# Kernel tuning notes

Hardware: AMD Instinct MI355X
Metric: run time of the kernel (lower is better)

Reference implementation:

```python
import jax, jax.numpy as jnp
import numpy as np

HEAD_SIZE = 64
TOKEN_EMB = 768
BLOCK_SIZE = 4096


def setup_inputs() -> dict:
    key = jax.random.key(0)
    ks = jax.random.split(key, 7)
    s = 1.0 / np.sqrt(TOKEN_EMB)  # torch Linear default init scale
    x = jax.random.normal(ks[0], (4, BLOCK_SIZE, TOKEN_EMB), dtype=jnp.float32)
    Wk = jax.random.uniform(ks[1], (TOKEN_EMB, HEAD_SIZE), minval=-s, maxval=s, dtype=jnp.float32)
    bk = jax.random.uniform(ks[2], (HEAD_SIZE,), minval=-s, maxval=s, dtype=jnp.float32)
    Wq = jax.random.uniform(ks[3], (TOKEN_EMB, HEAD_SIZE), minval=-s, maxval=s, dtype=jnp.float32)
    bq = jax.random.uniform(ks[4], (HEAD_SIZE,), minval=-s, maxval=s, dtype=jnp.float32)
    Wv = jax.random.uniform(ks[5], (TOKEN_EMB, HEAD_SIZE), minval=-s, maxval=s, dtype=jnp.float32)
    bv = jax.random.uniform(ks[6], (HEAD_SIZE,), minval=-s, maxval=s, dtype=jnp.float32)
    return {"x": x, "Wk": Wk, "bk": bk, "Wq": Wq, "bq": bq, "Wv": Wv, "bv": bv}


def reference(x, Wk, bk, Wq, bq, Wv, bv):
    B, T, C = x.shape
    k = x @ Wk + bk  # [B, T, H]
    q = x @ Wq + bq  # [B, T, H]
    v = x @ Wv + bv  # [B, T, H]
    # NOTE: original computes k @ q^T (not q @ k^T) and scales by C**-0.5 with
    # C = token embedding size (not head size). Reproduce faithfully.
    scale = jnp.asarray(C, x.dtype) ** -0.5
    wei = jnp.einsum('bth,bsh->bts', k, q) * scale  # [B, T, T]
    causal = jnp.tril(jnp.ones((T, T), dtype=bool))
    wei = jnp.where(causal, wei, -jnp.inf)
    wei = jax.nn.softmax(wei, axis=-1)
    return jnp.einsum('bts,bsh->bth', wei, v)  # [B, T, H]
```

## Files before the change

### kernel.cpp

```cpp
#include <hip/hip_runtime.h>
#include <hip/hip_bf16.h>

#define T_SEQ 4096
#define C_EMB 768
#define HEAD  64

typedef short  short4v __attribute__((ext_vector_type(4)));
typedef short  short8  __attribute__((ext_vector_type(8)));
typedef float  floatx4 __attribute__((ext_vector_type(4)));
typedef unsigned int uint2v __attribute__((ext_vector_type(2)));

static __device__ __forceinline__ short f2bf(float v) {
    __hip_bfloat16 h = __float2bfloat16(v);
    return *reinterpret_cast<short*>(&h);
}


__global__ void wt_transpose_kernel(const float* __restrict__ Wk,
                                    const float* __restrict__ Wq,
                                    const float* __restrict__ Wv,
                                    short* __restrict__ Wf) {
    const int total = 12 * 24 * 64 * 8;
    for (int idx = blockIdx.x * blockDim.x + threadIdx.x; idx < total;
         idx += gridDim.x * blockDim.x) {
        int e    = idx & 7;
        int lane = (idx >> 3) & 63;
        int t    = idx >> 9;
        int kc   = t % 24;
        int j    = t / 24;
        int g    = j >> 2;
        int n    = (j & 3) * 16 + (lane & 15);
        int k    = kc * 32 + ((lane >> 4) & 3) * 8 + e;
        const float* W = (g == 0) ? Wk : (g == 1) ? Wq : Wv;
        Wf[idx] = f2bf(W[k * HEAD + n]);
    }
}

__global__ __launch_bounds__(512) void qkv_mfma(
    const float* __restrict__ x, const short* __restrict__ Wf,
    const float* __restrict__ bkp, const float* __restrict__ bqp,
    const float* __restrict__ bvp,
    short* __restrict__ Kf, short* __restrict__ Qf, short* __restrict__ Vf) {
    const float scale2 = 0.052058773f;
    __shared__ __align__(16) short xs[32][776];

    const int tid  = threadIdx.x;
    const int w    = tid >> 6;
    const int lane = tid & 63;
    const int ln15 = lane & 15, quad = lane >> 4;
    const int rows0 = blockIdx.x * 32;
    const int rw = (w & 1) * 16;
    const int jb = (w >> 1) * 3;

#pragma unroll
    for (int grp = 0; grp < 2; ++grp) {
        floatx4 stg[6];
#pragma unroll
        for (int i = 0; i < 6; ++i) {
            int o = (grp * 6 + i) * 2048 + tid * 4;
            int r = o / 768, col = o - r * 768;
            stg[i] = *(const floatx4*)(x + (size_t)(rows0 + r) * C_EMB + col);
        }
#pragma unroll
        for (int i = 0; i < 6; ++i) {
            int o = (grp * 6 + i) * 2048 + tid * 4;
            int r = o / 768, col = o - r * 768;
            unsigned p01, p23;
            asm("v_cvt_pk_bf16_f32 %0, %1, %2" : "=v"(p01) : "v"(stg[i][0]), "v"(stg[i][1]));
            asm("v_cvt_pk_bf16_f32 %0, %1, %2" : "=v"(p23) : "v"(stg[i][2]), "v"(stg[i][3]));
            *(uint2v*)&xs[r][col] = (uint2v){p01, p23};
        }
    }
    __syncthreads();

    const short* wp[3];
#pragma unroll
    for (int j0 = 0; j0 < 3; ++j0)
        wp[j0] = Wf + ((size_t)((jb + j0) * 24) * 64 + lane) * 8;

    floatx4 acc[3];
#pragma unroll
    for (int jj = 0; jj < 3; ++jj) acc[jj] = (floatx4){0.f, 0.f, 0.f, 0.f};

#pragma unroll
    for (int kc = 0; kc < 24; ++kc) {
        short8 a = *(const short8*)&xs[rw + ln15][kc * 32 + quad * 8];
        short8 wf[3];
#pragma unroll
        for (int jj = 0; jj < 3; ++jj)
            wf[jj] = *(const short8*)(wp[jj] + kc * 512);
#pragma unroll
        for (int jj = 0; jj < 3; ++jj)
            acc[jj] = __builtin_amdgcn_mfma_f32_16x16x32_bf16(a, wf[jj], acc[jj], 0, 0, 0);
    }
    __syncthreads();

    short* lds = &xs[0][0];
#pragma unroll
    for (int jj = 0; jj < 3; ++jj) {
        int j  = jb + jj;
        int g  = j >> 2;
        int nl = (j & 3) * 16 + ln15;
        float bias = (g == 0 ? bkp : g == 1 ? bqp : bvp)[nl];
#pragma unroll
        for (int r = 0; r < 4; ++r) {
            int rloc = rw + quad * 4 + r;
            float v = acc[jj][r] + bias;
            int off;
            short val;
            if (g == 2) {
                val = f2bf(v);
                off = 4096 + ((nl >> 4) << 9) +
                      ((((rloc >> 3) & 3) << 4) | (nl & 15)) * 8 + (rloc & 7);
            } else {
                val = (g == 0) ? f2bf(v * scale2) : f2bf(v);
                int tr = rloc & 15, kh = nl >> 5;
                int hq = (nl >> 3) & 3, he = nl & 7;
                off = (g << 11) + (((rloc >> 4) * 2 + kh) << 9) +
                      (tr | (hq << 4)) * 8 + he;
            }
            lds[off] = val;
        }
    }
    __syncthreads();

    {
        int bb = rows0 >> 12, s = rows0 & 4095;
        size_t vbase = ((size_t)bb << 18) +
                       ((size_t)((s >> 6) * 8 + ((s >> 5) & 1)) << 9);
#pragma unroll
        for (int cc = 0; cc < 2; ++cc) {
            int i = (cc * 512 + tid) * 8;
            if (i < 6144) {
                short8 d = *(const short8*)&lds[i];
                if (i < 2048)
                    *(short8*)(Kf + (size_t)rows0 * 64 + i) = d;
                else if (i < 4096)
                    *(short8*)(Qf + (size_t)rows0 * 64 + (i - 2048)) = d;
                else {
                    int iv = i - 4096;
                    *(short8*)(Vf + vbase + (size_t)(iv >> 9) * 1024 + (iv & 511)) = d;
                }
            }
        }
    }
}

__global__ __launch_bounds__(64) void attn_part(
    const short* __restrict__ Kf, const short* __restrict__ Qf,
    const short* __restrict__ Vf, float* __restrict__ Opart,
    float* __restrict__ lpart) {
    __shared__ __align__(16) short Ps[32][72];

    int lane = threadIdx.x & 63;
    int ln15 = lane & 15, quad = lane >> 4;
    int g32 = blockIdx.x, c = blockIdx.y, b = blockIdx.z;
    int dtile = g32 >> 1;
    int lo = c * 8;
    if (lo > dtile) return;
    int hi = min(dtile, lo + 7);
    int base = g32 * 32;

    short8 bk[2][2];
    {
        const short* kfp = Kf + ((size_t)(b * 256 + g32 * 2) * 2) * 512 + lane * 8;
#pragma unroll
        for (int tg = 0; tg < 2; ++tg)
#pragma unroll
            for (int kh = 0; kh < 2; ++kh)
                bk[tg][kh] = *(const short8*)(kfp + (tg * 2 + kh) * 512);
    }

    floatx4 o[2][4];
#pragma unroll
    for (int tg = 0; tg < 2; ++tg)
#pragma unroll
        for (int hb = 0; hb < 4; ++hb) o[tg][hb] = (floatx4){0.f, 0.f, 0.f, 0.f};
    float ls[2] = {0.f, 0.f};

    const short* qfp = Qf + ((size_t)(b * 256 + lo * 4) * 2) * 512 + lane * 8;
    const short* vfp = Vf + ((size_t)b << 18) + (size_t)lo * 8 * 512 + lane * 8;

    short8 aqA[4][2], bvA[4][2], aqB[4][2], bvB[4][2];
#pragma unroll
    for (int sb = 0; sb < 4; ++sb)
#pragma unroll
        for (int kh = 0; kh < 2; ++kh)
            aqA[sb][kh] = *(const short8*)(qfp + (sb * 2 + kh) * 512);
#pragma unroll
    for (int hb = 0; hb < 4; ++hb)
#pragma unroll
        for (int kh = 0; kh < 2; ++kh)
            bvA[hb][kh] = *(const short8*)(vfp + (hb * 2 + kh) * 512);

    auto tile_step = [&](short8 (&aq)[4][2], short8 (&bv)[4][2],
                         short8 (&aqn)[4][2], short8 (&bvn)[4][2], int st) {
        if (st < hi) {
            int ti = st + 1 - lo;
#pragma unroll
            for (int sb = 0; sb < 4; ++sb)
#pragma unroll
                for (int kh = 0; kh < 2; ++kh)
                    aqn[sb][kh] = *(const short8*)(qfp + (size_t)ti * 4096 +
                                                   (sb * 2 + kh) * 512);
#pragma unroll
            for (int hb = 0; hb < 4; ++hb)
#pragma unroll
                for (int kh = 0; kh < 2; ++kh)
                    bvn[hb][kh] = *(const short8*)(vfp + (size_t)ti * 4096 +
                                                   (hb * 2 + kh) * 512);
        }

        floatx4 sacc[4][2];
#pragma unroll
        for (int sb = 0; sb < 4; ++sb)
#pragma unroll
            for (int tg = 0; tg < 2; ++tg) {
                floatx4 z = (floatx4){0.f, 0.f, 0.f, 0.f};
                z = __builtin_amdgcn_mfma_f32_16x16x32_bf16(aq[sb][0], bk[tg][0], z, 0, 0, 0);
                z = __builtin_amdgcn_mfma_f32_16x16x32_bf16(aq[sb][1], bk[tg][1], z, 0, 0, 0);
                sacc[sb][tg] = z;
            }

        bool diag = (st == dtile);
        int s0 = st * 64;
#pragma unroll
        for (int tg = 0; tg < 2; ++tg) {
            int tgl = base + tg * 16 + ln15;
#pragma unroll
            for (int sb = 0; sb < 4; ++sb) {
                float pv4[4];
#pragma unroll
                for (int r = 0; r < 4; ++r) {
                    float p = __builtin_amdgcn_exp2f(sacc[sb][tg][r]);
                    if (diag) {
                        int sg = s0 + sb * 16 + quad * 4 + r;
                        p = (sg > tgl) ? 0.f : p;
                    }
                    pv4[r] = p;
                }
                ls[tg] += (pv4[0] + pv4[1]) + (pv4[2] + pv4[3]);
                unsigned a01, a23;
                asm("v_cvt_pk_bf16_f32 %0, %1, %2" : "=v"(a01) : "v"(pv4[0]), "v"(pv4[1]));
                asm("v_cvt_pk_bf16_f32 %0, %1, %2" : "=v"(a23) : "v"(pv4[2]), "v"(pv4[3]));
                *(uint2v*)&Ps[tg * 16 + ln15][sb * 16 + quad * 4] = (uint2v){a01, a23};
            }
        }
        __asm__ volatile("s_waitcnt lgkmcnt(0)" ::: "memory");
        short8 ap[2][2];
#pragma unroll
        for (int tg = 0; tg < 2; ++tg) {
            ap[tg][0] = *(const short8*)&Ps[tg * 16 + ln15][quad * 8];
            ap[tg][1] = *(const short8*)&Ps[tg * 16 + ln15][32 + quad * 8];
        }

#pragma unroll
        for (int tg = 0; tg < 2; ++tg)
#pragma unroll
            for (int hb = 0; hb < 4; ++hb) {
                o[tg][hb] = __builtin_amdgcn_mfma_f32_16x16x32_bf16(ap[tg][0], bv[hb][0], o[tg][hb], 0, 0, 0);
                o[tg][hb] = __builtin_amdgcn_mfma_f32_16x16x32_bf16(ap[tg][1], bv[hb][1], o[tg][hb], 0, 0, 0);
            }
    };

#pragma unroll
    for (int it = 0; it < 8; it += 2) {
        if (lo + it > hi) break;
        tile_step(aqA, bvA, aqB, bvB, lo + it);
        if (lo + it + 1 > hi) break;
        tile_step(aqB, bvB, aqA, bvA, lo + it + 1);
    }

    float* op = Opart + ((size_t)(b * 8 + c) << 12) * HEAD;
    float* lp = lpart + ((size_t)(b * 8 + c) << 12);

#pragma unroll
    for (int tg = 0; tg < 2; ++tg) {
        float v = ls[tg];
        v += __shfl_xor(v, 16, 64);
        v += __shfl_xor(v, 32, 64);
        if (quad == 0)
            lp[base + tg * 16 + ln15] = v;
    }
#pragma unroll
    for (int tg = 0; tg < 2; ++tg)
#pragma unroll
        for (int r = 0; r < 4; ++r) {
            int t = base + tg * 16 + quad * 4 + r;
#pragma unroll
            for (int hb = 0; hb < 4; ++hb)
                op[(size_t)t * HEAD + hb * 16 + ln15] = o[tg][hb][r];
        }
}

__global__ __launch_bounds__(256) void attn_div(
    const float* __restrict__ Opart, const float* __restrict__ lpart,
    float* __restrict__ out) {
    int idx = blockIdx.x * 256 + threadIdx.x;
    int h = idx & 63;
    int t = (idx >> 6) & 4095;
    int b = idx >> 18;
    int nch = (t >> 9) + 1;
    float os = 0.f, l = 0.f;
    for (int c = 0; c < nch; ++c) {
        size_t s = (size_t)(b * 8 + c) << 12;
        os += Opart[(s + t) * HEAD + h];
        l  += lpart[s + t];
    }
    out[idx] = os / l;
}

extern "C" void kernel_launch(void* const* d_in, const int* in_sizes, int n_in,
                              void* d_out, int out_size, void* d_ws, size_t ws_size,
                              hipStream_t stream) {
    const int XSZ = 4 * T_SEQ * C_EMB;
    const int WSZ = C_EMB * HEAD;
    const int BSZ = HEAD;
    const float* x = nullptr;
    const float* W[3] = {nullptr, nullptr, nullptr};
    const float* B[3] = {nullptr, nullptr, nullptr};
    int iw = 0, ib = 0;
    for (int i = 0; i < n_in; ++i) {
        if (in_sizes[i] == XSZ) x = (const float*)d_in[i];
        else if (in_sizes[i] == WSZ && iw < 3) W[iw++] = (const float*)d_in[i];
        else if (in_sizes[i] == BSZ && ib < 3) B[ib++] = (const float*)d_in[i];
    }

    short* ws = (short*)d_ws;
    short* Kf = ws;
    short* Qf = Kf + (size_t)4 * T_SEQ * HEAD;
    short* Vf = Qf + (size_t)4 * T_SEQ * HEAD;
    short* Wf = Vf + (size_t)4 * HEAD * T_SEQ;
    float* Opart = (float*)(Wf + (size_t)3 * HEAD * C_EMB);
    float* lpart = Opart + (size_t)32 * T_SEQ * HEAD;

    wt_transpose_kernel<<<96, 256, 0, stream>>>(W[0], W[1], W[2], Wf);
    qkv_mfma<<<512, 512, 0, stream>>>(x, Wf, B[0], B[1], B[2], Kf, Qf, Vf);
    attn_part<<<dim3(128, 8, 4), 64, 0, stream>>>(Kf, Qf, Vf, Opart, lpart);
    attn_div<<<4096, 256, 0, stream>>>(Opart, lpart, (float*)d_out);
}
```

Measured before the change: 142.2 us.

## Split attention into 16 key chunks and drop register double-buffering

Halves the key-chunk size per attention workgroup (4 tiles instead of 8) and doubles the grid along the chunk axis, so more single-wave workgroups run in parallel and each finishes sooner. The manual ping-pong prefetch of Q/V fragments is replaced by a plain loop that loads each tile's fragments just before use. The reduction kernel now sums up to 16 partials per row, which doubles the partial-output workspace and the traffic through attn_div. Removing the prefetch may expose global load latency, but it lowers register pressure.

Result: faster. 137.2 us (-3.5%).

```diff
diff --git a/kernel.cpp b/kernel.cpp
--- a/kernel.cpp
+++ b/kernel.cpp
@@ -156,9 +156,9 @@
     int ln15 = lane & 15, quad = lane >> 4;
     int g32 = blockIdx.x, c = blockIdx.y, b = blockIdx.z;
     int dtile = g32 >> 1;
-    int lo = c * 8;
+    int lo = c * 4;
     if (lo > dtile) return;
-    int hi = min(dtile, lo + 7);
+    int hi = min(dtile, lo + 3);
     int base = g32 * 32;
 
     short8 bk[2][2];
@@ -181,35 +181,18 @@
     const short* qfp = Qf + ((size_t)(b * 256 + lo * 4) * 2) * 512 + lane * 8;
     const short* vfp = Vf + ((size_t)b << 18) + (size_t)lo * 8 * 512 + lane * 8;
 
-    short8 aqA[4][2], bvA[4][2], aqB[4][2], bvB[4][2];
-#pragma unroll
-    for (int sb = 0; sb < 4; ++sb)
-#pragma unroll
-        for (int kh = 0; kh < 2; ++kh)
-            aqA[sb][kh] = *(const short8*)(qfp + (sb * 2 + kh) * 512);
-#pragma unroll
-    for (int hb = 0; hb < 4; ++hb)
-#pragma unroll
-        for (int kh = 0; kh < 2; ++kh)
-            bvA[hb][kh] = *(const short8*)(vfp + (hb * 2 + kh) * 512);
-
-    auto tile_step = [&](short8 (&aq)[4][2], short8 (&bv)[4][2],
-                         short8 (&aqn)[4][2], short8 (&bvn)[4][2], int st) {
-        if (st < hi) {
-            int ti = st + 1 - lo;
-#pragma unroll
-            for (int sb = 0; sb < 4; ++sb)
-#pragma unroll
-                for (int kh = 0; kh < 2; ++kh)
-                    aqn[sb][kh] = *(const short8*)(qfp + (size_t)ti * 4096 +
-                                                   (sb * 2 + kh) * 512);
-#pragma unroll
-            for (int hb = 0; hb < 4; ++hb)
-#pragma unroll
-                for (int kh = 0; kh < 2; ++kh)
-                    bvn[hb][kh] = *(const short8*)(vfp + (size_t)ti * 4096 +
-                                                   (hb * 2 + kh) * 512);
-        }
+    for (int st = lo; st <= hi; ++st) {
+        short8 aq[4][2], bv[4][2];
+#pragma unroll
+        for (int sb = 0; sb < 4; ++sb)
+#pragma unroll
+            for (int kh = 0; kh < 2; ++kh)
+                aq[sb][kh] = *(const short8*)(qfp + (sb * 2 + kh) * 512);
+#pragma unroll
+        for (int hb = 0; hb < 4; ++hb)
+#pragma unroll
+            for (int kh = 0; kh < 2; ++kh)
+                bv[hb][kh] = *(const short8*)(vfp + (hb * 2 + kh) * 512);
 
         floatx4 sacc[4][2];
 #pragma unroll
@@ -261,18 +244,13 @@
                 o[tg][hb] = __builtin_amdgcn_mfma_f32_16x16x32_bf16(ap[tg][0], bv[hb][0], o[tg][hb], 0, 0, 0);
                 o[tg][hb] = __builtin_amdgcn_mfma_f32_16x16x32_bf16(ap[tg][1], bv[hb][1], o[tg][hb], 0, 0, 0);
             }
-    };
-
-#pragma unroll
-    for (int it = 0; it < 8; it += 2) {
-        if (lo + it > hi) break;
-        tile_step(aqA, bvA, aqB, bvB, lo + it);
-        if (lo + it + 1 > hi) break;
-        tile_step(aqB, bvB, aqA, bvA, lo + it + 1);
-    }
-
-    float* op = Opart + ((size_t)(b * 8 + c) << 12) * HEAD;
-    float* lp = lpart + ((size_t)(b * 8 + c) << 12);
+
+        qfp += 8 * 512;
+        vfp += 8 * 512;
+    }
+
+    float* op = Opart + ((size_t)(b * 16 + c) << 12) * HEAD;
+    float* lp = lpart + ((size_t)(b * 16 + c) << 12);
 
 #pragma unroll
     for (int tg = 0; tg < 2; ++tg) {
@@ -300,10 +278,10 @@
     int h = idx & 63;
     int t = (idx >> 6) & 4095;
     int b = idx >> 18;
-    int nch = (t >> 9) + 1;
+    int nch = (t >> 8) + 1;
     float os = 0.f, l = 0.f;
     for (int c = 0; c < nch; ++c) {
-        size_t s = (size_t)(b * 8 + c) << 12;
+        size_t s = (size_t)(b * 16 + c) << 12;
         os += Opart[(s + t) * HEAD + h];
         l  += lpart[s + t];
     }
@@ -332,10 +310,10 @@
     short* Vf = Qf + (size_t)4 * T_SEQ * HEAD;
     short* Wf = Vf + (size_t)4 * HEAD * T_SEQ;
     float* Opart = (float*)(Wf + (size_t)3 * HEAD * C_EMB);
-    float* lpart = Opart + (size_t)32 * T_SEQ * HEAD;
+    float* lpart = Opart + (size_t)64 * T_SEQ * HEAD;
 
     wt_transpose_kernel<<<96, 256, 0, stream>>>(W[0], W[1], W[2], Wf);
     qkv_mfma<<<512, 512, 0, stream>>>(x, Wf, B[0], B[1], B[2], Kf, Qf, Vf);
-    attn_part<<<dim3(128, 8, 4), 64, 0, stream>>>(Kf, Qf, Vf, Opart, lpart);
+    attn_part<<<dim3(128, 16, 4), 64, 0, stream>>>(Kf, Qf, Vf, Opart, lpart);
     attn_div<<<4096, 256, 0, stream>>>(Opart, lpart, (float*)d_out);
 }
```
